# Kernel tuning notes

Hardware: AMD Instinct MI355X
Metric: run time of the kernel (lower is better)

## Reference

```python
import jax, jax.numpy as jnp
import numpy as np

N_NODES = 50000
N_EDGES = 800000
A_DIM = 128
B_DIM = 128


def setup_inputs() -> dict:
    key = jax.random.key(0)
    k1, k2, k3, k4, k5, k6 = jax.random.split(key, 6)
    edge_rows = jax.random.randint(k1, (N_EDGES,), 0, N_NODES, dtype=jnp.int32)
    edge_cols = jax.random.randint(k2, (N_EDGES,), 0, N_NODES, dtype=jnp.int32)
    edge_vals = jax.random.uniform(k3, (N_EDGES,), dtype=jnp.float32)
    H = jax.random.normal(k4, (N_NODES, A_DIM), dtype=jnp.float32)
    std = 1.0 / np.sqrt(B_DIM)
    W = jax.random.uniform(k5, (A_DIM, B_DIM), minval=-std, maxval=std, dtype=jnp.float32)
    bias = jax.random.uniform(k6, (B_DIM,), minval=-std, maxval=std, dtype=jnp.float32)
    return {"edge_rows": edge_rows, "edge_cols": edge_cols, "edge_vals": edge_vals,
            "H": H, "W": W, "bias": bias}


def reference(edge_rows, edge_cols, edge_vals, H, W, bias):
    # HW = H @ W  (dense GEMM)
    HW = jnp.matmul(H, W)  # [n, b]
    # AHW = A @ HW where A is sparse COO: A[r, c] = v
    msgs = edge_vals[:, None] * HW[edge_cols]  # [nnz, b]
    AHW = jax.ops.segment_sum(msgs, edge_rows, num_segments=H.shape[0])  # [n, b]
    return AHW + bias
```

## Files before the change

### kernel.cpp

```cpp
#include <hip/hip_runtime.h>
#include <hip/hip_fp16.h>

#define ADIM 128
#define BDIM 128
#define CAP  64
#define NT   8
#define NKS  4

typedef _Float16 half8 __attribute__((ext_vector_type(8)));
typedef float    f32x4 __attribute__((ext_vector_type(4)));
typedef unsigned int uint;
typedef unsigned short ushort;

__global__ __launch_bounds__(256) void prep_kernel(const float* __restrict__ W,
                                                   _Float16* __restrict__ Bh,
                                                   _Float16* __restrict__ Bl,
                                                   int* __restrict__ counts,
                                                   int n_nodes) {
    const int gid = blockIdx.x * 256 + threadIdx.x;
    if (blockIdx.x < 8) {
        const int l  = gid & 63;
        const int ks = (gid >> 6) & 3;
        const int t  = gid >> 8;
        const int kbase = ks * 32 + (l >> 4) * 8;
        const int col   = t * 16 + (l & 15);
        half8 hi, lo;
#pragma unroll
        for (int j = 0; j < 8; ++j) {
            const float w = W[(size_t)(kbase + j) * BDIM + col];
            const _Float16 h = (_Float16)w;
            hi[j] = h;
            lo[j] = (_Float16)(w - (float)h);
        }
        const size_t off = ((size_t)(t * NKS + ks) * 64 + l) * 8;
        *(half8*)(Bh + off) = hi;
        *(half8*)(Bl + off) = lo;
    } else {
        const int idx = gid - 2048;
        if (idx < n_nodes) counts[idx] = 0;
    }
}

__global__ __launch_bounds__(256) void fused_gemm_bucket(
        const float* __restrict__ H,
        const _Float16* __restrict__ Bh, const _Float16* __restrict__ Bl,
        _Float16* __restrict__ HWh, int n_nodes, int gemm_blocks,
        const int* __restrict__ rows, const int* __restrict__ cols,
        const float* __restrict__ vals, int* __restrict__ counts,
        uint* __restrict__ ebuf, int n_edges) {
    const int tid = threadIdx.x;

    if ((int)blockIdx.x >= gemm_blocks) {
        const int e0 = ((int)blockIdx.x - gemm_blocks) * 512 + tid;
        const int e1 = e0 + 256;
        if (e0 < n_edges) {
            const int r = rows[e0];
            const int pos = atomicAdd(&counts[r], 1);
            if (pos < CAP)
                ebuf[(size_t)r * CAP + pos] =
                    ((uint)cols[e0] << 16) |
                    (uint)__half_as_ushort(__float2half(vals[e0]));
        }
        if (e1 < n_edges) {
            const int r = rows[e1];
            const int pos = atomicAdd(&counts[r], 1);
            if (pos < CAP)
                ebuf[(size_t)r * CAP + pos] =
                    ((uint)cols[e1] << 16) |
                    (uint)__half_as_ushort(__float2half(vals[e1]));
        }
        return;
    }

    const int l     = tid & 63;
    const int w     = tid >> 6;
    const int row_m = l & 15;
    const int kq    = l >> 4;
    const int n_strips = n_nodes >> 4;

    const int s0 = (int)blockIdx.x * 8 + w * 2;
    const bool ok0 = (s0 + 0) < n_strips;
    const bool ok1 = (s0 + 1) < n_strips;
    const int r0 = (s0 + 0) << 4;
    const int r1 = (s0 + 1) << 4;

    f32x4 acc[2][NT];
#pragma unroll
    for (int i = 0; i < 2; ++i)
#pragma unroll
        for (int t = 0; t < NT; ++t) acc[i][t] = (f32x4){0.f, 0.f, 0.f, 0.f};

#pragma unroll
    for (int ks = 0; ks < NKS; ++ks) {
        half8 ah[2], al[2];
#pragma unroll
        for (int i = 0; i < 2; ++i) {
            const bool ok = i ? ok1 : ok0;
            if (ok) {
                const int rr = (i ? r1 : r0) + row_m;
                const float4 x =
                    *(const float4*)(H + (size_t)rr * ADIM + ks * 32 + kq * 8);
                const float4 y =
                    *(const float4*)(H + (size_t)rr * ADIM + ks * 32 + kq * 8 + 4);
                const float xv[8] = {x.x, x.y, x.z, x.w, y.x, y.y, y.z, y.w};
#pragma unroll
                for (int j = 0; j < 8; ++j) {
                    const _Float16 h = (_Float16)xv[j];
                    ah[i][j] = h;
                    al[i][j] = (_Float16)(xv[j] - (float)h);
                }
            }
        }
#pragma unroll
        for (int t = 0; t < NT; ++t) {
            const size_t off = ((size_t)(t * NKS + ks) * 64 + l) * 8;
            const half8 bh = *(const half8*)(Bh + off);
            const half8 bl = *(const half8*)(Bl + off);
            if (ok0) {
                acc[0][t] = __builtin_amdgcn_mfma_f32_16x16x32_f16(ah[0], bh, acc[0][t], 0, 0, 0);
                acc[0][t] = __builtin_amdgcn_mfma_f32_16x16x32_f16(ah[0], bl, acc[0][t], 0, 0, 0);
                acc[0][t] = __builtin_amdgcn_mfma_f32_16x16x32_f16(al[0], bh, acc[0][t], 0, 0, 0);
            }
            if (ok1) {
                acc[1][t] = __builtin_amdgcn_mfma_f32_16x16x32_f16(ah[1], bh, acc[1][t], 0, 0, 0);
                acc[1][t] = __builtin_amdgcn_mfma_f32_16x16x32_f16(ah[1], bl, acc[1][t], 0, 0, 0);
                acc[1][t] = __builtin_amdgcn_mfma_f32_16x16x32_f16(al[1], bh, acc[1][t], 0, 0, 0);
            }
        }
    }

#pragma unroll
    for (int i = 0; i < 2; ++i) {
        const bool ok = i ? ok1 : ok0;
        if (!ok) continue;
        const int rb = (i ? r1 : r0) + kq * 4;
#pragma unroll
        for (int t = 0; t < NT; ++t)
#pragma unroll
            for (int r = 0; r < 4; ++r)
                HWh[(size_t)(rb + r) * BDIM + t * 16 + row_m] =
                    (_Float16)acc[i][t][r];
    }
}

__global__ __launch_bounds__(256) void gather_kernel(const int* __restrict__ counts,
                                                     const uint* __restrict__ ebuf,
                                                     const _Float16* __restrict__ HWh,
                                                     const float* __restrict__ bias,
                                                     float* __restrict__ out,
                                                     int n_nodes) {
    const int lane = threadIdx.x & 63;
    const int q    = lane >> 4;
    const int t    = lane & 15;
    const int node = (int)((blockIdx.x * (long)blockDim.x + threadIdx.x) >> 6);
    if (node >= n_nodes) return;

    int deg = __builtin_amdgcn_readfirstlane(counts[node]);
    if (deg > CAP) deg = CAP;

    const uint* ebn = ebuf + (size_t)node * CAP;

    float acc[8];
#pragma unroll
    for (int j = 0; j < 8; ++j) acc[j] = 0.f;

    for (int i = 0; i < deg; i += 8) {
        const int  ia = i + q;
        const int  ib = i + 4 + q;
        const bool oa = ia < deg;
        const bool ob = ib < deg;
        const uint ea = oa ? ebn[ia] : 0u;
        const uint eb = ob ? ebn[ib] : 0u;
        __half_raw hra, hrb;
        hra.x = (ushort)(ea & 0xFFFFu);
        hrb.x = (ushort)(eb & 0xFFFFu);
        const float va = oa ? __half2float(*(__half*)&hra) : 0.f;
        const float vb = ob ? __half2float(*(__half*)&hrb) : 0.f;
        const int4 ha = *(const int4*)(HWh + (size_t)(ea >> 16) * BDIM + t * 8);
        const int4 hb = *(const int4*)(HWh + (size_t)(eb >> 16) * BDIM + t * 8);

        const __half2* hpa = (const __half2*)&ha;
        const __half2* hpb = (const __half2*)&hb;
#pragma unroll
        for (int j = 0; j < 4; ++j) {
            const float2 fa = __half22float2(hpa[j]);
            acc[2 * j + 0] += fa.x * va;
            acc[2 * j + 1] += fa.y * va;
        }
#pragma unroll
        for (int j = 0; j < 4; ++j) {
            const float2 fb = __half22float2(hpb[j]);
            acc[2 * j + 0] += fb.x * vb;
            acc[2 * j + 1] += fb.y * vb;
        }
    }

#pragma unroll
    for (int j = 0; j < 8; ++j) {
        acc[j] += __shfl_xor(acc[j], 16, 64);
        acc[j] += __shfl_xor(acc[j], 32, 64);
    }

    if (q < 2) {
        const float4 b = ((const float4*)bias)[t * 2 + q];
        const float4 o = make_float4(acc[4 * q + 0] + b.x, acc[4 * q + 1] + b.y,
                                     acc[4 * q + 2] + b.z, acc[4 * q + 3] + b.w);
        *(float4*)(out + (size_t)node * BDIM + t * 8 + q * 4) = o;
    }
}

extern "C" void kernel_launch(void* const* d_in, const int* in_sizes, int n_in,
                              void* d_out, int out_size, void* d_ws, size_t ws_size,
                              hipStream_t stream) {
    const int*   edge_rows = (const int*)d_in[0];
    const int*   edge_cols = (const int*)d_in[1];
    const float* edge_vals = (const float*)d_in[2];
    const float* H         = (const float*)d_in[3];
    const float* W         = (const float*)d_in[4];
    const float* bias      = (const float*)d_in[5];

    const int n_edges = in_sizes[0];
    const int n_nodes = in_sizes[3] / ADIM;

    const size_t hw_bytes   = ((size_t)n_nodes * BDIM * sizeof(_Float16) + 15) & ~(size_t)15;
    const size_t cnt_bytes  = ((size_t)n_nodes * sizeof(int) + 15) & ~(size_t)15;
    const size_t ebuf_bytes = ((size_t)n_nodes * CAP * sizeof(uint) + 15) & ~(size_t)15;
    const size_t frag_bytes = (size_t)NT * NKS * 64 * 8 * sizeof(_Float16);

    char* ws = (char*)d_ws;
    _Float16* HWh  = (_Float16*)ws;  ws += hw_bytes;
    int*      cnt  = (int*)ws;       ws += cnt_bytes;
    uint*     ebuf = (uint*)ws;      ws += ebuf_bytes;
    _Float16* Bh   = (_Float16*)ws;  ws += frag_bytes;
    _Float16* Bl   = (_Float16*)ws;

    const int zero_blocks = (n_nodes + 255) / 256;
    prep_kernel<<<8 + zero_blocks, 256, 0, stream>>>(W, Bh, Bl, cnt, n_nodes);

    const int n_strips     = n_nodes >> 4;
    const int gemm_blocks  = (n_strips + 7) / 8;
    const int bucket_blocks = (n_edges + 511) / 512;
    fused_gemm_bucket<<<gemm_blocks + bucket_blocks, 256, 0, stream>>>(
        H, Bh, Bl, HWh, n_nodes, gemm_blocks,
        edge_rows, edge_cols, edge_vals, cnt, ebuf, n_edges);

    gather_kernel<<<(n_nodes + 3) / 4, 256, 0, stream>>>(cnt, ebuf, HWh, bias,
                                                         (float*)d_out, n_nodes);
}
```

Baseline: 162.2 us.

## Split fused GEMM/bucket kernel, vectorize edge bucketing, deepen gather loads

The fused GEMM-plus-bucketing kernel is split into two separate launches. The bucketing kernel now handles four edges per thread using vectorized int4/float4 loads. The gather loop is restructured to issue four independent HWh row loads per lane per iteration (16 edges per wave step instead of 8), which raises memory-level parallelism. This gives up any overlap between GEMM and bucketing blocks inside one launch and adds one kernel launch.

```diff
diff --git a/kernel.cpp b/kernel.cpp
--- a/kernel.cpp
+++ b/kernel.cpp
@@ -41,37 +41,11 @@
     }
 }
 
-__global__ __launch_bounds__(256) void fused_gemm_bucket(
+__global__ __launch_bounds__(256) void gemm_kernel(
         const float* __restrict__ H,
         const _Float16* __restrict__ Bh, const _Float16* __restrict__ Bl,
-        _Float16* __restrict__ HWh, int n_nodes, int gemm_blocks,
-        const int* __restrict__ rows, const int* __restrict__ cols,
-        const float* __restrict__ vals, int* __restrict__ counts,
-        uint* __restrict__ ebuf, int n_edges) {
-    const int tid = threadIdx.x;
-
-    if ((int)blockIdx.x >= gemm_blocks) {
-        const int e0 = ((int)blockIdx.x - gemm_blocks) * 512 + tid;
-        const int e1 = e0 + 256;
-        if (e0 < n_edges) {
-            const int r = rows[e0];
-            const int pos = atomicAdd(&counts[r], 1);
-            if (pos < CAP)
-                ebuf[(size_t)r * CAP + pos] =
-                    ((uint)cols[e0] << 16) |
-                    (uint)__half_as_ushort(__float2half(vals[e0]));
-        }
-        if (e1 < n_edges) {
-            const int r = rows[e1];
-            const int pos = atomicAdd(&counts[r], 1);
-            if (pos < CAP)
-                ebuf[(size_t)r * CAP + pos] =
-                    ((uint)cols[e1] << 16) |
-                    (uint)__half_as_ushort(__float2half(vals[e1]));
-        }
-        return;
-    }
-
+        _Float16* __restrict__ HWh, int n_nodes) {
+    const int tid   = threadIdx.x;
     const int l     = tid & 63;
     const int w     = tid >> 6;
     const int row_m = l & 15;
@@ -140,6 +114,43 @@
             for (int r = 0; r < 4; ++r)
                 HWh[(size_t)(rb + r) * BDIM + t * 16 + row_m] =
                     (_Float16)acc[i][t][r];
+    }
+}
+
+__global__ __launch_bounds__(256) void bucket_kernel(const int* __restrict__ rows,
+                                                     const int* __restrict__ cols,
+                                                     const float* __restrict__ vals,
+                                                     int* __restrict__ counts,
+                                                     uint* __restrict__ ebuf,
+                                                     int n_edges) {
+    const int g4 = blockIdx.x * 256 + threadIdx.x;
+    const int e0 = g4 * 4;
+    if (e0 >= n_edges) return;
+
+    if (e0 + 4 <= n_edges) {
+        const int4   r4 = *(const int4*)(rows + e0);
+        const int4   c4 = *(const int4*)(cols + e0);
+        const float4 v4 = *(const float4*)(vals + e0);
+        const int   rr[4] = {r4.x, r4.y, r4.z, r4.w};
+        const int   cc[4] = {c4.x, c4.y, c4.z, c4.w};
+        const float vv[4] = {v4.x, v4.y, v4.z, v4.w};
+#pragma unroll
+        for (int u = 0; u < 4; ++u) {
+            const int pos = atomicAdd(&counts[rr[u]], 1);
+            if (pos < CAP)
+                ebuf[(size_t)rr[u] * CAP + pos] =
+                    ((uint)cc[u] << 16) |
+                    (uint)__half_as_ushort(__float2half(vv[u]));
+        }
+    } else {
+        for (int e = e0; e < n_edges; ++e) {
+            const int r = rows[e];
+            const int pos = atomicAdd(&counts[r], 1);
+            if (pos < CAP)
+                ebuf[(size_t)r * CAP + pos] =
+                    ((uint)cols[e] << 16) |
+                    (uint)__half_as_ushort(__float2half(vals[e]));
+        }
     }
 }
 
@@ -164,34 +175,28 @@
 #pragma unroll
     for (int j = 0; j < 8; ++j) acc[j] = 0.f;
 
-    for (int i = 0; i < deg; i += 8) {
-        const int  ia = i + q;
-        const int  ib = i + 4 + q;
-        const bool oa = ia < deg;
-        const bool ob = ib < deg;
-        const uint ea = oa ? ebn[ia] : 0u;
-        const uint eb = ob ? ebn[ib] : 0u;
-        __half_raw hra, hrb;
-        hra.x = (ushort)(ea & 0xFFFFu);
-        hrb.x = (ushort)(eb & 0xFFFFu);
-        const float va = oa ? __half2float(*(__half*)&hra) : 0.f;
-        const float vb = ob ? __half2float(*(__half*)&hrb) : 0.f;
-        const int4 ha = *(const int4*)(HWh + (size_t)(ea >> 16) * BDIM + t * 8);
-        const int4 hb = *(const int4*)(HWh + (size_t)(eb >> 16) * BDIM + t * 8);
-
-        const __half2* hpa = (const __half2*)&ha;
-        const __half2* hpb = (const __half2*)&hb;
-#pragma unroll
-        for (int j = 0; j < 4; ++j) {
-            const float2 fa = __half22float2(hpa[j]);
-            acc[2 * j + 0] += fa.x * va;
-            acc[2 * j + 1] += fa.y * va;
-        }
-#pragma unroll
-        for (int j = 0; j < 4; ++j) {
-            const float2 fb = __half22float2(hpb[j]);
-            acc[2 * j + 0] += fb.x * vb;
-            acc[2 * j + 1] += fb.y * vb;
+    for (int i0 = 0; i0 < deg; i0 += 16) {
+        uint e[4];
+#pragma unroll
+        for (int u = 0; u < 4; ++u) {
+            const int idx = i0 + q + 4 * u;
+            e[u] = (idx < deg) ? ebn[idx] : 0u;
+        }
+        int4 h[4];
+#pragma unroll
+        for (int u = 0; u < 4; ++u)
+            h[u] = *(const int4*)(HWh + (size_t)(e[u] >> 16) * BDIM + t * 8);
+#pragma unroll
+        for (int u = 0; u < 4; ++u) {
+            __half_raw hr; hr.x = (ushort)(e[u] & 0xFFFFu);
+            const float v = __half2float(*(__half*)&hr);
+            const __half2* hp = (const __half2*)&h[u];
+#pragma unroll
+            for (int j = 0; j < 4; ++j) {
+                const float2 f = __half22float2(hp[j]);
+                acc[2 * j + 0] += f.x * v;
+                acc[2 * j + 1] += f.y * v;
+            }
         }
     }
 
@@ -237,12 +242,13 @@
     const int zero_blocks = (n_nodes + 255) / 256;
     prep_kernel<<<8 + zero_blocks, 256, 0, stream>>>(W, Bh, Bl, cnt, n_nodes);
 
-    const int n_strips     = n_nodes >> 4;
-    const int gemm_blocks  = (n_strips + 7) / 8;
-    const int bucket_blocks = (n_edges + 511) / 512;
-    fused_gemm_bucket<<<gemm_blocks + bucket_blocks, 256, 0, stream>>>(
-        H, Bh, Bl, HWh, n_nodes, gemm_blocks,
-        edge_rows, edge_cols, edge_vals, cnt, ebuf, n_edges);
+    const int bucket_blocks = (n_edges + 1023) / 1024;
+    bucket_kernel<<<bucket_blocks, 256, 0, stream>>>(edge_rows, edge_cols,
+                                                     edge_vals, cnt, ebuf, n_edges);
+
+    const int n_strips    = n_nodes >> 4;
+    const int gemm_blocks = (n_strips + 7) / 8;
+    gemm_kernel<<<gemm_blocks, 256, 0, stream>>>(H, Bh, Bl, HWh, n_nodes);
 
     gather_kernel<<<(n_nodes + 3) / 4, 256, 0, stream>>>(cnt, ebuf, HWh, bias,
                                                          (float*)d_out, n_nodes);
```

After: 184.9 us. 13.9% more time.
